# Optimization experiments

Measured on AMD Instinct MI355X. Metric: run time of the kernel, lower is better.

Reference implementation:

```python
import jax, jax.numpy as jnp
import numpy as np

N_NODES = 50000
N_EDGES = 800000
EMB = 384
HID = 64
HEADS = 4


def setup_inputs() -> dict:
    key = jax.random.key(0)
    ks = jax.random.split(key, 16)
    g = lambda k, shape, scale: jax.random.normal(k, shape, jnp.float32) * scale
    node_feats = jax.random.normal(ks[0], (N_NODES, EMB), jnp.float32)
    edge_index = jax.random.randint(ks[1], (2, N_EDGES), 0, N_NODES, jnp.int32)
    return dict(
        node_feats=node_feats,
        edge_index=edge_index,
        # GAT layer 1: 384 -> 4 heads x 64
        W1=g(ks[2], (EMB, HEADS * HID), 1.0 / np.sqrt(EMB)),
        att_src1=g(ks[3], (HEADS, HID), 1.0 / np.sqrt(HID)),
        att_dst1=g(ks[4], (HEADS, HID), 1.0 / np.sqrt(HID)),
        b1=jnp.zeros((HEADS * HID,), jnp.float32),
        # GAT layer 2: 256 -> 1 head x 64
        W2=g(ks[5], (HEADS * HID, HID), 1.0 / np.sqrt(HEADS * HID)),
        att_src2=g(ks[6], (1, HID), 1.0 / np.sqrt(HID)),
        att_dst2=g(ks[7], (1, HID), 1.0 / np.sqrt(HID)),
        b2=jnp.zeros((HID,), jnp.float32),
        # Attentional pooling gate MLP: 64 -> 64 -> 1
        gate_W1=g(ks[8], (HID, HID), 1.0 / np.sqrt(HID)),
        gate_b1=jnp.zeros((HID,), jnp.float32),
        gate_W2=g(ks[9], (HID, 1), 1.0 / np.sqrt(HID)),
        gate_b2=jnp.zeros((1,), jnp.float32),
    )


def _segment_softmax(logits, seg, n):
    # logits: (E, H); softmax over edges sharing the same destination node.
    m = jax.ops.segment_max(logits, seg, num_segments=n)
    m = jnp.where(jnp.isfinite(m), m, 0.0)  # guard empty segments
    e = jnp.exp(logits - m[seg])
    s = jax.ops.segment_sum(e, seg, num_segments=n)
    return e / (s[seg] + 1e-16)


def _gat(x, src, dst, W, a_s, a_d, b, heads, ch):
    # PyG GATConv: shared linear, per-head additive attention, LeakyReLU(0.2),
    # dst-segment softmax, scatter-sum, concat heads, + bias.
    n = x.shape[0]
    h = (x @ W).reshape(n, heads, ch)                    # (N,H,C)
    al_s = jnp.einsum('nhc,hc->nh', h, a_s)              # (N,H)
    al_d = jnp.einsum('nhc,hc->nh', h, a_d)
    e = jax.nn.leaky_relu(al_s[src] + al_d[dst], 0.2)    # (E,H)
    alpha = _segment_softmax(e, dst, n)                  # (E,H)
    out = jax.ops.segment_sum(h[src] * alpha[:, :, None], dst, num_segments=n)
    return out.reshape(n, heads * ch) + b


def reference(node_feats, edge_index, W1, att_src1, att_dst1, b1,
              W2, att_src2, att_dst2, b2,
              gate_W1, gate_b1, gate_W2, gate_b2):
    n = node_feats.shape[0]
    loops = jnp.arange(n, dtype=edge_index.dtype)        # GATConv add_self_loops=True
    src = jnp.concatenate([edge_index[0], loops])
    dst = jnp.concatenate([edge_index[1], loops])
    x = jax.nn.elu(_gat(node_feats, src, dst, W1, att_src1, att_dst1, b1, HEADS, HID))
    x = jax.nn.elu(_gat(x, src, dst, W2, att_src2, att_dst2, b2, 1, HID))
    # AttentionalAggregation over a single graph (index all zeros):
    gate = jax.nn.relu(x @ gate_W1 + gate_b1) @ gate_W2 + gate_b2  # (N,1)
    w = jax.nn.softmax(gate, axis=0)
    return (w * x).sum(axis=0, keepdims=True)            # (1, HID)
```

## Files before the change

kernel.cpp:

```cpp
#include <hip/hip_runtime.h>
#include <hip/hip_bf16.h>
#include <math.h>

#define N_NODES 50000
#define N_EDGES 800000
#define E_TOT   (N_EDGES + N_NODES)
#define EMB     384
#define HID     64
#define HEADS   4
#define C1      (HEADS * HID)
#define CHUNK   256

typedef unsigned short u16;
typedef __attribute__((ext_vector_type(8))) short bf16x8;
typedef __attribute__((ext_vector_type(4))) float f32x4;

__device__ __forceinline__ u16 f2b(float x) {
    unsigned u = __float_as_uint(x);
    return (u16)((u + 0x7FFFu + ((u >> 16) & 1u)) >> 16);
}
__device__ __forceinline__ float b2f(u16 h) {
    return __uint_as_float(((unsigned)h) << 16);
}

__device__ __forceinline__ unsigned fkey(float f) {
    unsigned b = __float_as_uint(f);
    return (b & 0x80000000u) ? ~b : (b | 0x80000000u);
}
__device__ __forceinline__ float funkey(unsigned u) {
    return (u & 0x80000000u) ? __uint_as_float(u ^ 0x80000000u)
                             : __uint_as_float(~u);
}

__device__ __forceinline__ void edge_sd(int e, const int* __restrict__ ei,
                                        int& s, int& d) {
    if (e < N_EDGES) { s = ei[e]; d = ei[N_EDGES + e]; }
    else             { s = d = e - N_EDGES; }
}

__global__ __launch_bounds__(256) void deg_kernel(const int* __restrict__ ei,
                                                  int* __restrict__ deg) {
    const int e = blockIdx.x * 256 + threadIdx.x;
    if (e >= E_TOT) return;
    int s, d; edge_sd(e, ei, s, d);
    atomicAdd(&deg[d], 1);
}

__global__ __launch_bounds__(1024) void scan_kernel(const int* __restrict__ deg,
                                                    int* __restrict__ rowptr) {
    __shared__ int ts[1024];
    const int t  = threadIdx.x;
    const int CH = (N_NODES + 1023) / 1024;
    const int st = t * CH;
    const int en = st + CH < N_NODES ? st + CH : N_NODES;
    int s = 0;
    for (int i = st; i < en; ++i) s += deg[i];
    ts[t] = s;
    __syncthreads();
    for (int off = 1; off < 1024; off <<= 1) {
        int v = (t >= off) ? ts[t - off] : 0;
        __syncthreads();
        ts[t] += v;
        __syncthreads();
    }
    int off = ts[t] - s;
    for (int i = st; i < en; ++i) { rowptr[i] = off; off += deg[i]; }
}

__global__ __launch_bounds__(256) void fill_kernel(const int* __restrict__ ei,
                                                   const int* __restrict__ rowptr,
                                                   int* __restrict__ cursor,
                                                   int* __restrict__ csr) {
    const int e = blockIdx.x * 256 + threadIdx.x;
    if (e >= E_TOT) return;
    int s, d; edge_sd(e, ei, s, d);
    int p = atomicAdd(&cursor[d], 1);
    csr[rowptr[d] + p] = s;
}

__global__ __launch_bounds__(256) void conv_w_kernel(
        const float* __restrict__ W1, const float* __restrict__ W2,
        u16* __restrict__ W1t, u16* __restrict__ W2t) {
    const int i = blockIdx.x * 256 + threadIdx.x;
    if (i < EMB * C1) {
        int k = i >> 8, c = i & 255;
        W1t[c * EMB + k] = f2b(W1[i]);
    }
    if (i < C1 * HID) {
        int k = i >> 6, c = i & 63;
        W2t[c * C1 + k] = f2b(W2[i]);
    }
}

__global__ __launch_bounds__(256) void gemm1_mfma(
        const float* __restrict__ X, const u16* __restrict__ W1t,
        u16* __restrict__ Hb) {
    __shared__ u16 As[64][40];
    const int r0 = blockIdx.x * 64;
    const int w  = threadIdx.x >> 6;
    const int l  = threadIdx.x & 63;
    const int lr = l & 15, lg = l >> 4;
    f32x4 acc[4][4] = {};
    for (int k0 = 0; k0 < EMB; k0 += 32) {
        __syncthreads();
#pragma unroll
        for (int it = 0; it < 2; ++it) {
            int i   = threadIdx.x + it * 256;
            int row = i >> 3, kq = (i & 7) * 4;
            int grow = r0 + row;
            float4 v = (grow < N_NODES)
                ? *(const float4*)&X[(size_t)grow * EMB + k0 + kq]
                : make_float4(0.f, 0.f, 0.f, 0.f);
            uint2 p;
            p.x = (unsigned)f2b(v.x) | ((unsigned)f2b(v.y) << 16);
            p.y = (unsigned)f2b(v.z) | ((unsigned)f2b(v.w) << 16);
            *(uint2*)&As[row][kq] = p;
        }
        __syncthreads();
        const u16* wp = W1t + (size_t)(w * 64 + lr) * EMB + k0 + lg * 8;
        bf16x8 bfr[4], afr[4];
        bfr[0] = *(const bf16x8*)(wp);
        bfr[1] = *(const bf16x8*)(wp + 16 * EMB);
        bfr[2] = *(const bf16x8*)(wp + 32 * EMB);
        bfr[3] = *(const bf16x8*)(wp + 48 * EMB);
#pragma unroll
        for (int rt = 0; rt < 4; ++rt)
            afr[rt] = *(const bf16x8*)&As[rt * 16 + lr][lg * 8];
#pragma unroll
        for (int rt = 0; rt < 4; ++rt)
#pragma unroll
            for (int ct = 0; ct < 4; ++ct)
                acc[rt][ct] = __builtin_amdgcn_mfma_f32_16x16x32_bf16(
                    afr[rt], bfr[ct], acc[rt][ct], 0, 0, 0);
    }
#pragma unroll
    for (int rt = 0; rt < 4; ++rt)
#pragma unroll
        for (int reg = 0; reg < 4; ++reg) {
            int row = r0 + rt * 16 + lg * 4 + reg;
            if (row < N_NODES) {
#pragma unroll
                for (int ct = 0; ct < 4; ++ct)
                    Hb[(size_t)row * C1 + w * 64 + ct * 16 + lr] =
                        f2b(acc[rt][ct][reg]);
            }
        }
}

__global__ __launch_bounds__(256) void gemm2_mfma(
        const u16* __restrict__ Xb, const u16* __restrict__ W2t,
        u16* __restrict__ Hb) {
    __shared__ u16 As[64][40];
    const int r0 = blockIdx.x * 64;
    const int w  = threadIdx.x >> 6;
    const int l  = threadIdx.x & 63;
    const int lr = l & 15, lg = l >> 4;
    f32x4 acc[4] = {};
    for (int k0 = 0; k0 < C1; k0 += 32) {
        __syncthreads();
        {
            int i   = threadIdx.x;
            int row = i >> 2, kq = (i & 3) * 8;
            int grow = r0 + row;
            uint4 v = (grow < N_NODES)
                ? *(const uint4*)&Xb[(size_t)grow * C1 + k0 + kq]
                : make_uint4(0u, 0u, 0u, 0u);
            *(uint4*)&As[row][kq] = v;
        }
        __syncthreads();
        bf16x8 bfr = *(const bf16x8*)&W2t[(size_t)(w * 16 + lr) * C1 + k0 + lg * 8];
#pragma unroll
        for (int rt = 0; rt < 4; ++rt) {
            bf16x8 afr = *(const bf16x8*)&As[rt * 16 + lr][lg * 8];
            acc[rt] = __builtin_amdgcn_mfma_f32_16x16x32_bf16(
                afr, bfr, acc[rt], 0, 0, 0);
        }
    }
#pragma unroll
    for (int rt = 0; rt < 4; ++rt)
#pragma unroll
        for (int reg = 0; reg < 4; ++reg) {
            int row = r0 + rt * 16 + lg * 4 + reg;
            if (row < N_NODES)
                Hb[(size_t)row * HID + w * 16 + lr] = f2b(acc[rt][reg]);
        }
}

__global__ __launch_bounds__(256) void al1_kernel(
        const u16* __restrict__ Hb, const float* __restrict__ as_,
        const float* __restrict__ ad_, float* __restrict__ als,
        float* __restrict__ ald) {
    const int n = blockIdx.x;
    const int h = threadIdx.x >> 6;
    const int c = threadIdx.x & 63;
    float v = b2f(Hb[(size_t)n * C1 + h * HID + c]);
    float s = v * as_[h * HID + c];
    float d = v * ad_[h * HID + c];
#pragma unroll
    for (int off = 32; off > 0; off >>= 1) {
        s += __shfl_down(s, off);
        d += __shfl_down(d, off);
    }
    if (c == 0) { als[n * HEADS + h] = s; ald[n * HEADS + h] = d; }
}

__global__ __launch_bounds__(256) void al2_kernel(
        const u16* __restrict__ Hb, const float* __restrict__ as_,
        const float* __restrict__ ad_, float* __restrict__ als,
        float* __restrict__ ald) {
    const int n = blockIdx.x * 4 + (threadIdx.x >> 6);
    const int c = threadIdx.x & 63;
    float v = b2f(Hb[(size_t)n * HID + c]);
    float s = v * as_[c];
    float d = v * ad_[c];
#pragma unroll
    for (int off = 32; off > 0; off >>= 1) {
        s += __shfl_down(s, off);
        d += __shfl_down(d, off);
    }
    if (c == 0) { als[n] = s; ald[n] = d; }
}

__global__ __launch_bounds__(256) void agg1_kernel(
        const int* __restrict__ csr, const int* __restrict__ rowptr,
        const int* __restrict__ deg, const u16* __restrict__ Hb,
        const float* __restrict__ als, const float* __restrict__ ald,
        float* __restrict__ xout) {
    __shared__ float alpha_s[CHUNK][5];
    __shared__ int   src_s[CHUNK];
    __shared__ float red_s[4][C1];
    const int d = blockIdx.x;
    const int w = threadIdx.x >> 6;
    const int c = threadIdx.x & 63;
    const int row = rowptr[d];
    const int dg  = deg[d];
    const float aldv = ald[d * HEADS + w];
    float lmax = -1e30f;
    for (int j = c; j < dg; j += 64) {
        int s = csr[row + j];
        float l = als[s * HEADS + w] + aldv;
        l = l > 0.f ? l : 0.2f * l;
        lmax = fmaxf(lmax, l);
    }
#pragma unroll
    for (int off = 32; off > 0; off >>= 1)
        lmax = fmaxf(lmax, __shfl_xor(lmax, off));
    float lsum = 0.f;
    for (int j = c; j < dg; j += 64) {
        int s = csr[row + j];
        float l = als[s * HEADS + w] + aldv;
        l = l > 0.f ? l : 0.2f * l;
        lsum += expf(l - lmax);
    }
#pragma unroll
    for (int off = 32; off > 0; off >>= 1) lsum += __shfl_xor(lsum, off);
    const float inv = 1.f / (lsum + 1e-16f);

    float4 acc = make_float4(0.f, 0.f, 0.f, 0.f);
    const int myh = c >> 4;
    for (int base = 0; base < dg; base += CHUNK) {
        const int cn = (dg - base) < CHUNK ? (dg - base) : CHUNK;
        for (int j = c; j < cn; j += 64) {
            int s = csr[row + base + j];
            if (w == 0) src_s[j] = s;
            float l = als[s * HEADS + w] + aldv;
            l = l > 0.f ? l : 0.2f * l;
            alpha_s[j][w] = expf(l - lmax) * inv;
        }
        __syncthreads();
        for (int j = w; j < cn; j += 4) {
            int s = src_s[j];
            float a = alpha_s[j][myh];
            uint2 v = *(const uint2*)&Hb[(size_t)s * C1 + c * 4];
            acc.x = fmaf(a, __uint_as_float(v.x << 16), acc.x);
            acc.y = fmaf(a, __uint_as_float(v.x & 0xFFFF0000u), acc.y);
            acc.z = fmaf(a, __uint_as_float(v.y << 16), acc.z);
            acc.w = fmaf(a, __uint_as_float(v.y & 0xFFFF0000u), acc.w);
        }
        __syncthreads();
    }
    *(float4*)&red_s[w][c * 4] = acc;
    __syncthreads();
    float r = red_s[0][threadIdx.x] + red_s[1][threadIdx.x] +
              red_s[2][threadIdx.x] + red_s[3][threadIdx.x];
    xout[(size_t)d * C1 + threadIdx.x] = r;
}

__global__ __launch_bounds__(256) void agg2_kernel(
        const int* __restrict__ csr, const int* __restrict__ rowptr,
        const int* __restrict__ deg, const u16* __restrict__ Hb,
        const float* __restrict__ als, const float* __restrict__ ald,
        float* __restrict__ xout) {
    __shared__ float alpha_s[CHUNK];
    __shared__ int   src_s[CHUNK];
    __shared__ float red_s[4][HID];
    const int d = blockIdx.x;
    const int w = threadIdx.x >> 6;
    const int c = threadIdx.x & 63;
    const int row = rowptr[d];
    const int dg  = deg[d];
    const float aldv = ald[d];
    float lmax = -1e30f;
    for (int j = c; j < dg; j += 64) {
        int s = csr[row + j];
        float l = als[s] + aldv;
        l = l > 0.f ? l : 0.2f * l;
        lmax = fmaxf(lmax, l);
    }
#pragma unroll
    for (int off = 32; off > 0; off >>= 1)
        lmax = fmaxf(lmax, __shfl_xor(lmax, off));
    float lsum = 0.f;
    for (int j = c; j < dg; j += 64) {
        int s = csr[row + j];
        float l = als[s] + aldv;
        l = l > 0.f ? l : 0.2f * l;
        lsum += expf(l - lmax);
    }
#pragma unroll
    for (int off = 32; off > 0; off >>= 1) lsum += __shfl_xor(lsum, off);
    const float inv = 1.f / (lsum + 1e-16f);

    float acc = 0.f;
    for (int base = 0; base < dg; base += CHUNK) {
        const int cn = (dg - base) < CHUNK ? (dg - base) : CHUNK;
        for (int j = threadIdx.x; j < cn; j += 256) {
            int s = csr[row + base + j];
            src_s[j] = s;
            float l = als[s] + aldv;
            l = l > 0.f ? l : 0.2f * l;
            alpha_s[j] = expf(l - lmax) * inv;
        }
        __syncthreads();
        for (int j = w; j < cn; j += 4)
            acc = fmaf(alpha_s[j], b2f(Hb[(size_t)src_s[j] * HID + c]), acc);
        __syncthreads();
    }
    red_s[w][c] = acc;
    __syncthreads();
    if (threadIdx.x < HID) {
        float r = red_s[0][threadIdx.x] + red_s[1][threadIdx.x] +
                  red_s[2][threadIdx.x] + red_s[3][threadIdx.x];
        xout[(size_t)d * HID + threadIdx.x] = r;
    }
}

__global__ __launch_bounds__(256) void elu1_kernel(
        const float* __restrict__ x, const float* __restrict__ b,
        u16* __restrict__ xb) {
    const size_t i = (size_t)blockIdx.x * 256 + threadIdx.x;
    float v = x[i] + b[i & 255];
    v = v > 0.f ? v : expm1f(v);
    xb[i] = f2b(v);
}

__global__ __launch_bounds__(256) void elu2_kernel(float* __restrict__ x,
                                                   const float* __restrict__ b) {
    const size_t i = (size_t)blockIdx.x * 256 + threadIdx.x;
    float v = x[i] + b[i & 63];
    x[i] = v > 0.f ? v : expm1f(v);
}

__global__ __launch_bounds__(256) void gate_kernel(
        const float* __restrict__ x2, const float* __restrict__ gW1,
        const float* __restrict__ gb1, const float* __restrict__ gW2,
        const float* __restrict__ gb2, float* __restrict__ gate) {
    const int n = blockIdx.x * 4 + (threadIdx.x >> 6);
    const int c = threadIdx.x & 63;
    const float* xr = x2 + (size_t)n * HID;
    float acc = 0.f;
    for (int k = 0; k < HID; ++k) acc = fmaf(xr[k], gW1[k * HID + c], acc);
    float t = acc + gb1[c];
    t = t > 0.f ? t : 0.f;
    float g = t * gW2[c];
#pragma unroll
    for (int off = 32; off > 0; off >>= 1) g += __shfl_down(g, off);
    if (c == 0) gate[n] = g + gb2[0];
}

__global__ __launch_bounds__(256) void gmax_kernel(
        const float* __restrict__ gate, unsigned* __restrict__ gmax) {
    float m = -1e30f;
    for (int n = blockIdx.x * 256 + threadIdx.x; n < N_NODES;
         n += gridDim.x * 256)
        m = fmaxf(m, gate[n]);
    __shared__ float red[256];
    red[threadIdx.x] = m;
    __syncthreads();
    for (int s = 128; s > 0; s >>= 1) {
        if (threadIdx.x < s)
            red[threadIdx.x] = fmaxf(red[threadIdx.x], red[threadIdx.x + s]);
        __syncthreads();
    }
    if (threadIdx.x == 0) atomicMax(gmax, fkey(red[0]));
}

__global__ __launch_bounds__(256) void egate_kernel(
        float* __restrict__ gate, const unsigned* __restrict__ gmax,
        float* __restrict__ gsum) {
    const int n = blockIdx.x * 256 + threadIdx.x;
    float e = 0.f;
    if (n < N_NODES) {
        float m = funkey(*gmax);
        e = expf(gate[n] - m);
        gate[n] = e;
    }
    __shared__ float red[256];
    red[threadIdx.x] = e;
    __syncthreads();
    for (int s = 128; s > 0; s >>= 1) {
        if (threadIdx.x < s) red[threadIdx.x] += red[threadIdx.x + s];
        __syncthreads();
    }
    if (threadIdx.x == 0) atomicAdd(gsum, red[0]);
}

__global__ __launch_bounds__(256) void final_kernel(
        const float* __restrict__ x2, const float* __restrict__ egate,
        const float* __restrict__ gsum, float* __restrict__ out) {
    const int c   = threadIdx.x & 63;
    const int sub = threadIdx.x >> 6;
    float acc = 0.f;
    for (int n = blockIdx.x * 4 + sub; n < N_NODES; n += gridDim.x * 4)
        acc += egate[n] * x2[(size_t)n * HID + c];
    __shared__ float red[256];
    red[threadIdx.x] = acc;
    __syncthreads();
    if (threadIdx.x < 64) {
        float t = red[threadIdx.x] + red[64 + threadIdx.x] +
                  red[128 + threadIdx.x] + red[192 + threadIdx.x];
        atomicAdd(&out[c], t / (*gsum));
    }
}

extern "C" void kernel_launch(void* const* d_in, const int* in_sizes, int n_in,
                              void* d_out, int out_size, void* d_ws, size_t ws_size,
                              hipStream_t stream) {
    const float* node_feats = (const float*)d_in[0];
    const int*   ei         = (const int*)d_in[1];
    const float* W1   = (const float*)d_in[2];
    const float* as1  = (const float*)d_in[3];
    const float* ad1  = (const float*)d_in[4];
    const float* b1   = (const float*)d_in[5];
    const float* W2   = (const float*)d_in[6];
    const float* as2  = (const float*)d_in[7];
    const float* ad2  = (const float*)d_in[8];
    const float* b2   = (const float*)d_in[9];
    const float* gW1  = (const float*)d_in[10];
    const float* gb1  = (const float*)d_in[11];
    const float* gW2  = (const float*)d_in[12];
    const float* gb2  = (const float*)d_in[13];
    float* out = (float*)d_out;

    float* f = (float*)d_ws;
    size_t o = 0;
    float* x1   = f + o; o += (size_t)N_NODES * C1;
    float* x2   = f + o; o += (size_t)N_NODES * HID;
    float* als1 = f + o; o += (size_t)N_NODES * HEADS;
    float* ald1 = f + o; o += (size_t)N_NODES * HEADS;
    float* als2 = f + o; o += N_NODES;
    float* ald2 = f + o; o += N_NODES;
    float* gate = f + o; o += N_NODES;
    int* csr    = (int*)(f + o); o += E_TOT;
    int* rowptr = (int*)(f + o); o += N_NODES;
    u16* h1b    = (u16*)(f + o); o += (size_t)N_NODES * C1 / 2;
    u16* x1b    = (u16*)(f + o); o += (size_t)N_NODES * C1 / 2;
    u16* h2b    = (u16*)(f + o); o += (size_t)N_NODES * HID / 2;
    u16* W1t    = (u16*)(f + o); o += (size_t)EMB * C1 / 2;
    u16* W2t    = (u16*)(f + o); o += (size_t)C1 * HID / 2;
    float* zero0 = f + o;
    int* deg    = (int*)(f + o); o += N_NODES;
    int* cursor = (int*)(f + o); o += N_NODES;
    float* scal = f + o; o += 2;
    size_t zbytes = (size_t)((f + o) - zero0) * sizeof(float);

    hipMemsetAsync(zero0, 0, zbytes, stream);
    hipMemsetAsync(out, 0, (size_t)out_size * sizeof(float), stream);

    const int EB = (E_TOT + 255) / 256;
    const int GB = (N_NODES + 63) / 64;

    conv_w_kernel<<<(EMB * C1 + 255) / 256, 256, 0, stream>>>(W1, W2, W1t, W2t);
    deg_kernel<<<EB, 256, 0, stream>>>(ei, deg);
    scan_kernel<<<1, 1024, 0, stream>>>(deg, rowptr);
    fill_kernel<<<EB, 256, 0, stream>>>(ei, rowptr, cursor, csr);

    gemm1_mfma<<<GB, 256, 0, stream>>>(node_feats, W1t, h1b);
    al1_kernel<<<N_NODES, 256, 0, stream>>>(h1b, as1, ad1, als1, ald1);
    agg1_kernel<<<N_NODES, 256, 0, stream>>>(csr, rowptr, deg, h1b, als1, ald1, x1);
    elu1_kernel<<<(N_NODES * C1) / 256, 256, 0, stream>>>(x1, b1, x1b);

    gemm2_mfma<<<GB, 256, 0, stream>>>(x1b, W2t, h2b);
    al2_kernel<<<N_NODES / 4, 256, 0, stream>>>(h2b, as2, ad2, als2, ald2);
    agg2_kernel<<<N_NODES, 256, 0, stream>>>(csr, rowptr, deg, h2b, als2, ald2, x2);
    elu2_kernel<<<(N_NODES * HID) / 256, 256, 0, stream>>>(x2, b2);

    gate_kernel<<<N_NODES / 4, 256, 0, stream>>>(x2, gW1, gb1, gW2, gb2, gate);
    gmax_kernel<<<48, 256, 0, stream>>>(gate, (unsigned*)&scal[0]);
    egate_kernel<<<(N_NODES + 255) / 256, 256, 0, stream>>>(
        gate, (const unsigned*)&scal[0], &scal[1]);
    final_kernel<<<256, 256, 0, stream>>>(x2, gate, &scal[1], out);
}
```

Baseline: 725.2 us.

## Use single-pass unnormalized softmax in GAT aggregation and fuse bias+ELU

```diff
diff --git a/kernel.cpp b/kernel.cpp
--- a/kernel.cpp
+++ b/kernel.cpp
@@ -225,39 +225,21 @@
         const int* __restrict__ csr, const int* __restrict__ rowptr,
         const int* __restrict__ deg, const u16* __restrict__ Hb,
         const float* __restrict__ als, const float* __restrict__ ald,
-        float* __restrict__ xout) {
+        const float* __restrict__ b1, u16* __restrict__ xb) {
     __shared__ float alpha_s[CHUNK][5];
     __shared__ int   src_s[CHUNK];
     __shared__ float red_s[4][C1];
+    __shared__ float lsum_s[4];
     const int d = blockIdx.x;
     const int w = threadIdx.x >> 6;
     const int c = threadIdx.x & 63;
     const int row = rowptr[d];
     const int dg  = deg[d];
     const float aldv = ald[d * HEADS + w];
-    float lmax = -1e30f;
-    for (int j = c; j < dg; j += 64) {
-        int s = csr[row + j];
-        float l = als[s * HEADS + w] + aldv;
-        l = l > 0.f ? l : 0.2f * l;
-        lmax = fmaxf(lmax, l);
-    }
-#pragma unroll
-    for (int off = 32; off > 0; off >>= 1)
-        lmax = fmaxf(lmax, __shfl_xor(lmax, off));
+    const int myh = c >> 4;
+
+    float4 acc = make_float4(0.f, 0.f, 0.f, 0.f);
     float lsum = 0.f;
-    for (int j = c; j < dg; j += 64) {
-        int s = csr[row + j];
-        float l = als[s * HEADS + w] + aldv;
-        l = l > 0.f ? l : 0.2f * l;
-        lsum += expf(l - lmax);
-    }
-#pragma unroll
-    for (int off = 32; off > 0; off >>= 1) lsum += __shfl_xor(lsum, off);
-    const float inv = 1.f / (lsum + 1e-16f);
-
-    float4 acc = make_float4(0.f, 0.f, 0.f, 0.f);
-    const int myh = c >> 4;
     for (int base = 0; base < dg; base += CHUNK) {
         const int cn = (dg - base) < CHUNK ? (dg - base) : CHUNK;
         for (int j = c; j < cn; j += 64) {
@@ -265,7 +247,9 @@
             if (w == 0) src_s[j] = s;
             float l = als[s * HEADS + w] + aldv;
             l = l > 0.f ? l : 0.2f * l;
-            alpha_s[j][w] = expf(l - lmax) * inv;
+            float p = expf(fminf(l, 60.f));
+            alpha_s[j][w] = p;
+            lsum += p;
         }
         __syncthreads();
         for (int j = w; j < cn; j += 4) {
@@ -279,49 +263,36 @@
         }
         __syncthreads();
     }
+#pragma unroll
+    for (int off = 32; off > 0; off >>= 1) lsum += __shfl_xor(lsum, off);
+    if (c == 0) lsum_s[w] = lsum;
     *(float4*)&red_s[w][c * 4] = acc;
     __syncthreads();
     float r = red_s[0][threadIdx.x] + red_s[1][threadIdx.x] +
               red_s[2][threadIdx.x] + red_s[3][threadIdx.x];
-    xout[(size_t)d * C1 + threadIdx.x] = r;
+    r = r / (lsum_s[w] + 1e-16f) + b1[threadIdx.x];
+    r = r > 0.f ? r : expm1f(r);
+    xb[(size_t)d * C1 + threadIdx.x] = f2b(r);
 }
 
 __global__ __launch_bounds__(256) void agg2_kernel(
         const int* __restrict__ csr, const int* __restrict__ rowptr,
         const int* __restrict__ deg, const u16* __restrict__ Hb,
         const float* __restrict__ als, const float* __restrict__ ald,
-        float* __restrict__ xout) {
+        const float* __restrict__ b2, float* __restrict__ xout) {
     __shared__ float alpha_s[CHUNK];
     __shared__ int   src_s[CHUNK];
     __shared__ float red_s[4][HID];
+    __shared__ float lsum_s[4];
     const int d = blockIdx.x;
     const int w = threadIdx.x >> 6;
     const int c = threadIdx.x & 63;
     const int row = rowptr[d];
     const int dg  = deg[d];
     const float aldv = ald[d];
-    float lmax = -1e30f;
-    for (int j = c; j < dg; j += 64) {
-        int s = csr[row + j];
-        float l = als[s] + aldv;
-        l = l > 0.f ? l : 0.2f * l;
-        lmax = fmaxf(lmax, l);
-    }
-#pragma unroll
-    for (int off = 32; off > 0; off >>= 1)
-        lmax = fmaxf(lmax, __shfl_xor(lmax, off));
+
+    float acc = 0.f;
     float lsum = 0.f;
-    for (int j = c; j < dg; j += 64) {
-        int s = csr[row + j];
-        float l = als[s] + aldv;
-        l = l > 0.f ? l : 0.2f * l;
-        lsum += expf(l - lmax);
-    }
-#pragma unroll
-    for (int off = 32; off > 0; off >>= 1) lsum += __shfl_xor(lsum, off);
-    const float inv = 1.f / (lsum + 1e-16f);
-
-    float acc = 0.f;
     for (int base = 0; base < dg; base += CHUNK) {
         const int cn = (dg - base) < CHUNK ? (dg - base) : CHUNK;
         for (int j = threadIdx.x; j < cn; j += 256) {
@@ -329,36 +300,28 @@
             src_s[j] = s;
             float l = als[s] + aldv;
             l = l > 0.f ? l : 0.2f * l;
-            alpha_s[j] = expf(l - lmax) * inv;
+            float p = expf(fminf(l, 60.f));
+            alpha_s[j] = p;
+            lsum += p;
         }
         __syncthreads();
         for (int j = w; j < cn; j += 4)
             acc = fmaf(alpha_s[j], b2f(Hb[(size_t)src_s[j] * HID + c]), acc);
         __syncthreads();
     }
+#pragma unroll
+    for (int off = 32; off > 0; off >>= 1) lsum += __shfl_xor(lsum, off);
+    if (c == 0) lsum_s[w] = lsum;
     red_s[w][c] = acc;
     __syncthreads();
     if (threadIdx.x < HID) {
+        float ls = lsum_s[0] + lsum_s[1] + lsum_s[2] + lsum_s[3];
         float r = red_s[0][threadIdx.x] + red_s[1][threadIdx.x] +
                   red_s[2][threadIdx.x] + red_s[3][threadIdx.x];
+        r = r / (ls + 1e-16f) + b2[threadIdx.x];
+        r = r > 0.f ? r : expm1f(r);
         xout[(size_t)d * HID + threadIdx.x] = r;
     }
-}
-
-__global__ __launch_bounds__(256) void elu1_kernel(
-        const float* __restrict__ x, const float* __restrict__ b,
-        u16* __restrict__ xb) {
-    const size_t i = (size_t)blockIdx.x * 256 + threadIdx.x;
-    float v = x[i] + b[i & 255];
-    v = v > 0.f ? v : expm1f(v);
-    xb[i] = f2b(v);
-}
-
-__global__ __launch_bounds__(256) void elu2_kernel(float* __restrict__ x,
-                                                   const float* __restrict__ b) {
-    const size_t i = (size_t)blockIdx.x * 256 + threadIdx.x;
-    float v = x[i] + b[i & 63];
-    x[i] = v > 0.f ? v : expm1f(v);
 }
 
 __global__ __launch_bounds__(256) void gate_kernel(
@@ -454,7 +417,6 @@
 
     float* f = (float*)d_ws;
     size_t o = 0;
-    float* x1   = f + o; o += (size_t)N_NODES * C1;
     float* x2   = f + o; o += (size_t)N_NODES * HID;
     float* als1 = f + o; o += (size_t)N_NODES * HEADS;
     float* ald1 = f + o; o += (size_t)N_NODES * HEADS;
@@ -487,13 +449,13 @@
 
     gemm1_mfma<<<GB, 256, 0, stream>>>(node_feats, W1t, h1b);
     al1_kernel<<<N_NODES, 256, 0, stream>>>(h1b, as1, ad1, als1, ald1);
-    agg1_kernel<<<N_NODES, 256, 0, stream>>>(csr, rowptr, deg, h1b, als1, ald1, x1);
-    elu1_kernel<<<(N_NODES * C1) / 256, 256, 0, stream>>>(x1, b1, x1b);
+    agg1_kernel<<<N_NODES, 256, 0, stream>>>(csr, rowptr, deg, h1b, als1, ald1,
+                                             b1, x1b);
 
     gemm2_mfma<<<GB, 256, 0, stream>>>(x1b, W2t, h2b);
     al2_kernel<<<N_NODES / 4, 256, 0, stream>>>(h2b, as2, ad2, als2, ald2);
-    agg2_kernel<<<N_NODES, 256, 0, stream>>>(csr, rowptr, deg, h2b, als2, ald2, x2);
-    elu2_kernel<<<(N_NODES * HID) / 256, 256, 0, stream>>>(x2, b2);
+    agg2_kernel<<<N_NODES, 256, 0, stream>>>(csr, rowptr, deg, h2b, als2, ald2,
+                                             b2, x2);
 
     gate_kernel<<<N_NODES / 4, 256, 0, stream>>>(x2, gW1, gb1, gW2, gb2, gate);
     gmax_kernel<<<48, 256, 0, stream>>>(gate, (unsigned*)&scal[0]);
```

Result: faster. 657.3 us (-9.4%).
